# Kernel optimization log

Measured on AMD Instinct MI355X. Metric: run time of the kernel, lower is better.

## Reference

```python
import jax, jax.numpy as jnp
import numpy as np

NUM_HEADS = 16
BN_EPS = 1e-5


def setup_inputs() -> dict:
    key = jax.random.key(0)
    ks = jax.random.split(key, 12)
    B, S, D = 8, 1024, 1024
    s = 1.0 / np.sqrt(D)
    return {
        "key": jax.random.normal(ks[0], (B, S, D), jnp.float32),
        "value": jax.random.normal(ks[1], (B, S, D), jnp.float32),
        "query": jax.random.normal(ks[2], (B, S, D), jnp.float32),
        "Wk": jax.random.normal(ks[3], (D, D), jnp.float32) * s,
        "bk": jax.random.normal(ks[4], (D,), jnp.float32) * s,
        "Wv": jax.random.normal(ks[5], (D, D), jnp.float32) * s,
        "bv": jax.random.normal(ks[6], (D,), jnp.float32) * s,
        "Wq": jax.random.normal(ks[7], (D, D), jnp.float32) * s,
        "bq": jax.random.normal(ks[8], (D,), jnp.float32) * s,
        "Wf": jax.random.normal(ks[9], (D, D), jnp.float32) * s,
        "bf": jax.random.normal(ks[10], (D,), jnp.float32) * s,
        "gamma": jnp.ones((D,), jnp.float32),
        "beta": jnp.zeros((D,), jnp.float32),
    }


def _mha(key, value, query, Wk, bk, Wv, bv, Wq, bq, Wf, bf, gamma, beta):
    B, S, D = query.shape
    H = NUM_HEADS
    d = D // H
    residual = query

    k = key @ Wk + bk      # [B, S, D]
    v = value @ Wv + bv
    q = query @ Wq + bq

    # Faithful to torch: raw row-major view(B*H, -1, d) — NOT the standard head transpose.
    k = k.reshape(B * H, -1, d)   # [B*H, S, d]
    v = v.reshape(B * H, -1, d)
    q = q.reshape(B * H, -1, d)

    # Faithful quirky scale: (dim_per_head // num_heads) ** -0.5
    scale = jnp.float32((d // H) ** (-0.5))

    scores = jnp.einsum('bqd,bkd->bqk', q, k) * scale          # [B*H, S, S]
    attention = jax.nn.softmax(scores, axis=2)
    context = jnp.einsum('bqk,bkd->bqd', attention, v)          # [B*H, S, d]

    context = context.reshape(B, -1, D)                         # [B, S, D]
    out = context @ Wf + bf

    # BatchNorm1d over channel dim D (training mode: batch stats over B and S, biased var)
    x = residual + out                                          # [B, S, D]
    mean = jnp.mean(x, axis=(0, 1))
    var = jnp.mean((x - mean) ** 2, axis=(0, 1))
    out = (x - mean) * jax.lax.rsqrt(var + BN_EPS) * gamma + beta
    return out, attention


def reference(key, value, query, Wk, bk, Wv, bv, Wq, bq, Wf, bf, gamma, beta):
    return _mha(key, value, query, Wk, bk, Wv, bv, Wq, bq, Wf, bf, gamma, beta)
```

## Files before the change

### kernel.cpp

```cpp
#include <hip/hip_runtime.h>
#include <hip/hip_bf16.h>
#include <stdint.h>

typedef __attribute__((ext_vector_type(8))) short     short8;
typedef __attribute__((ext_vector_type(8))) _Float16  f16x8;
typedef __attribute__((ext_vector_type(4))) float     f32x4;
typedef __attribute__((ext_vector_type(8))) unsigned short ushort8;
typedef __attribute__((ext_vector_type(4))) unsigned short ushort4_t;

__device__ inline unsigned short f2bf(float f) {
    unsigned u = __float_as_uint(f);
    u += 0x7fffu + ((u >> 16) & 1u);
    return (unsigned short)(u >> 16);
}
__device__ inline float bf2f(unsigned short h) {
    return __uint_as_float(((unsigned)h) << 16);
}
__device__ inline unsigned short f2h(float f) {
    _Float16 h = (_Float16)f;
    unsigned short r;
    __builtin_memcpy(&r, &h, 2);
    return r;
}

__device__ inline void gload16(const void* g, void* lds) {
    unsigned loff = (unsigned)(uintptr_t)lds;
    loff = __builtin_amdgcn_readfirstlane(loff);
    auto l = (__attribute__((address_space(3))) unsigned int*)(uintptr_t)loff;
    auto p = (const __attribute__((address_space(1))) unsigned int*)(uintptr_t)g;
    __builtin_amdgcn_global_load_lds(p, l, 16, 0, 0);
}

template<int TOF16>
__global__ void cvt_f32_2b(const float4* __restrict__ in, ushort4_t* __restrict__ out, int n4) {
    for (int i = blockIdx.x * blockDim.x + threadIdx.x; i < n4; i += gridDim.x * blockDim.x) {
        float4 v = in[i];
        ushort4_t r;
        if constexpr (TOF16) { r.x = f2h(v.x);  r.y = f2h(v.y);  r.z = f2h(v.z);  r.w = f2h(v.w); }
        else                 { r.x = f2bf(v.x); r.y = f2bf(v.y); r.z = f2bf(v.z); r.w = f2bf(v.w); }
        out[i] = r;
    }
}

template<int TOF16>
__global__ void transpose_cvt(const float* __restrict__ W, unsigned short* __restrict__ WT, int dim) {
    __shared__ float t[32][33];
    const int bx = blockIdx.x * 32, by = blockIdx.y * 32;
    const int tx = threadIdx.x, ty = threadIdx.y;
#pragma unroll
    for (int i = 0; i < 4; ++i)
        t[ty + 8 * i][tx] = W[(size_t)(by + ty + 8 * i) * dim + bx + tx];
    __syncthreads();
#pragma unroll
    for (int i = 0; i < 4; ++i) {
        float v = t[tx][ty + 8 * i];
        WT[(size_t)(bx + ty + 8 * i) * dim + by + tx] = TOF16 ? f2h(v) : f2bf(v);
    }
}

__global__ void transpose_v(const unsigned short* __restrict__ v, unsigned short* __restrict__ vT) {
    const int bh = blockIdx.z, d0 = blockIdx.x * 32, s0 = blockIdx.y * 32;
    __shared__ unsigned short t[32][33];
    const int tx = threadIdx.x, ty = threadIdx.y;
    const size_t base = (size_t)bh << 16;
#pragma unroll
    for (int i = 0; i < 4; ++i)
        t[ty + 8 * i][tx] = v[base + (size_t)(s0 + ty + 8 * i) * 64 + d0 + tx];
    __syncthreads();
#pragma unroll
    for (int i = 0; i < 4; ++i)
        vT[base + (size_t)(d0 + ty + 8 * i) * 1024 + s0 + tx] = t[tx][ty + 8 * i];
}

template<int F16IN, int EPI>
__global__ __launch_bounds__(256, 2) void gemm_bt(
    const unsigned short* __restrict__ A,
    const unsigned short* __restrict__ Bt,
    const float* __restrict__ bias,
    unsigned short* __restrict__ C2b,
    const float* __restrict__ resid,
    float* __restrict__ Cf,
    int M, int N, int K, int nbx)
{
    const int bid = blockIdx.x;
    const int cpx = gridDim.x >> 3;
    const int swz = (bid & 7) * cpx + (bid >> 3);
    const int bm = swz / nbx, bn = swz % nbx;
    const int m0 = bm * 128, n0 = bn * 128;

    const int tid = threadIdx.x;
    const int w = tid >> 6, l = tid & 63, g = l >> 4, c = l & 15;
    const int wr = w >> 1, wc = w & 1;

    __shared__ unsigned short As[4096];
    __shared__ unsigned short Bs[4096];

    f32x4 acc[4][4] = {};

    const int arow = tid >> 2, acol = (tid & 3) * 8;
    const unsigned short* Ap  = A  + (size_t)(m0 + arow) * K + acol;
    const unsigned short* Ap2 = A  + (size_t)(m0 + 64 + arow) * K + acol;
    const unsigned short* Bp  = Bt + (size_t)(n0 + arow) * K + acol;
    const unsigned short* Bp2 = Bt + (size_t)(n0 + 64 + arow) * K + acol;
    unsigned short* AsW  = &As[w * 512];
    unsigned short* AsW2 = &As[2048 + w * 512];
    unsigned short* BsW  = &Bs[w * 512];
    unsigned short* BsW2 = &Bs[2048 + w * 512];

    for (int k0 = 0; k0 < K; k0 += 32) {
        gload16(Ap + k0,  AsW);
        gload16(Ap2 + k0, AsW2);
        gload16(Bp + k0,  BsW);
        gload16(Bp2 + k0, BsW2);
        asm volatile("s_waitcnt vmcnt(0)" ::: "memory");
        __syncthreads();

        if constexpr (F16IN) {
            f16x8 a[4], b[4];
#pragma unroll
            for (int mt = 0; mt < 4; ++mt)
                a[mt] = *(const f16x8*)&As[(wr * 64 + mt * 16 + c) * 32 + g * 8];
#pragma unroll
            for (int nt = 0; nt < 4; ++nt)
                b[nt] = *(const f16x8*)&Bs[(wc * 64 + nt * 16 + c) * 32 + g * 8];
#pragma unroll
            for (int mt = 0; mt < 4; ++mt)
#pragma unroll
                for (int nt = 0; nt < 4; ++nt)
                    acc[mt][nt] = __builtin_amdgcn_mfma_f32_16x16x32_f16(a[mt], b[nt], acc[mt][nt], 0, 0, 0);
        } else {
            short8 a[4], b[4];
#pragma unroll
            for (int mt = 0; mt < 4; ++mt)
                a[mt] = *(const short8*)&As[(wr * 64 + mt * 16 + c) * 32 + g * 8];
#pragma unroll
            for (int nt = 0; nt < 4; ++nt)
                b[nt] = *(const short8*)&Bs[(wc * 64 + nt * 16 + c) * 32 + g * 8];
#pragma unroll
            for (int mt = 0; mt < 4; ++mt)
#pragma unroll
                for (int nt = 0; nt < 4; ++nt)
                    acc[mt][nt] = __builtin_amdgcn_mfma_f32_16x16x32_bf16(a[mt], b[nt], acc[mt][nt], 0, 0, 0);
        }
        __syncthreads();
    }

#pragma unroll
    for (int nt = 0; nt < 4; ++nt) {
        const int col = n0 + wc * 64 + nt * 16 + c;
        const float bs = bias[col];
#pragma unroll
        for (int mt = 0; mt < 4; ++mt) {
            const int row0 = m0 + wr * 64 + mt * 16 + g * 4;
#pragma unroll
            for (int r = 0; r < 4; ++r) {
                const float x = acc[mt][nt][r] + bs;
                const size_t idx = (size_t)(row0 + r) * N + col;
                if constexpr (EPI == 0) {
                    C2b[idx] = F16IN ? f2h(x) : f2bf(x);
                } else {
                    Cf[idx] = x + resid[idx];
                }
            }
        }
    }
}

__global__ __launch_bounds__(256, 4) void attn_kernel(
    const unsigned short* __restrict__ qf,
    const unsigned short* __restrict__ kf,
    const unsigned short* __restrict__ vT,
    float* __restrict__ attn_out,
    unsigned short* __restrict__ ctx)
{
    const int rb = blockIdx.x;
    const int bh = blockIdx.y;
    const int tid = threadIdx.x;
    const int w = tid >> 6, l = tid & 63, g = l >> 4, c = l & 15;
    const int n0 = w * 256;

    __shared__ unsigned short P[16 * 1024];
    __shared__ float rs_lds[4][16];
    __shared__ float inv_lds[16];

    const unsigned short* qb = qf + ((size_t)bh << 16) + (size_t)(rb * 16 + c) * 64 + g * 8;
    const f16x8 q0 = *(const f16x8*)(qb);
    const f16x8 q1 = *(const f16x8*)(qb + 32);

    const unsigned short* kb = kf + ((size_t)bh << 16);
    const unsigned swzc = ((unsigned)(c & 7)) << 4;
    const unsigned prow = (unsigned)c * 2048;

    f32x4 pt[16];
    float rsum = 0.f;

#pragma unroll
    for (int t = 0; t < 16; ++t) {
        const unsigned short* kp = kb + (size_t)(n0 + t * 16 + c) * 64 + g * 8;
        const f16x8 a0 = *(const f16x8*)(kp);
        const f16x8 a1 = *(const f16x8*)(kp + 32);
        f32x4 s = {0.f, 0.f, 0.f, 0.f};
        s = __builtin_amdgcn_mfma_f32_16x16x32_f16(a0, q0, s, 0, 0, 0);
        s = __builtin_amdgcn_mfma_f32_16x16x32_f16(a1, q1, s, 0, 0, 0);

        f32x4 p;
        p[0] = __expf(s[0] * 0.5f);
        p[1] = __expf(s[1] * 0.5f);
        p[2] = __expf(s[2] * 0.5f);
        p[3] = __expf(s[3] * 0.5f);
        pt[t] = p;
        rsum += (p[0] + p[1]) + (p[2] + p[3]);

        ushort4_t pk;
        pk.x = f2bf(p[0]); pk.y = f2bf(p[1]); pk.z = f2bf(p[2]); pk.w = f2bf(p[3]);
        *(ushort4_t*)((char*)P + ((prow + (unsigned)(n0 * 2 + t * 32 + g * 8)) ^ swzc)) = pk;
    }

    rsum += __shfl_xor(rsum, 16);
    rsum += __shfl_xor(rsum, 32);
    if (g == 0) rs_lds[w][c] = rsum;
    __syncthreads();
    if (tid < 16)
        inv_lds[tid] = 1.0f / (rs_lds[0][tid] + rs_lds[1][tid] + rs_lds[2][tid] + rs_lds[3][tid]);
    __syncthreads();

    const float inv = inv_lds[c];
    float* ao = attn_out + ((size_t)bh << 20) + (size_t)(rb * 16 + c) * 1024 + n0 + g * 4;
#pragma unroll
    for (int t = 0; t < 16; ++t) {
        f32x4 o;
        o[0] = pt[t][0] * inv;
        o[1] = pt[t][1] * inv;
        o[2] = pt[t][2] * inv;
        o[3] = pt[t][3] * inv;
        __builtin_nontemporal_store(o, (f32x4*)(ao + t * 16));
    }

    f32x4 pacc = {0.f, 0.f, 0.f, 0.f};
    const unsigned short* vb = vT + ((size_t)bh << 16) + (size_t)(w * 16 + c) * 1024;
#pragma unroll 4
    for (int ks = 0; ks < 32; ++ks) {
        const short8 a = *(const short8*)((char*)P + ((prow + (unsigned)(ks * 64 + g * 16)) ^ swzc));
        const short8 b = *(const short8*)(vb + ks * 32 + g * 8);
        pacc = __builtin_amdgcn_mfma_f32_16x16x32_bf16(a, b, pacc, 0, 0, 0);
    }
    unsigned short* cb = ctx + ((size_t)bh << 16) + (size_t)(rb * 16) * 64 + w * 16 + c;
#pragma unroll
    for (int r = 0; r < 4; ++r) {
        const int row = g * 4 + r;
        cb[(size_t)row * 64] = f2bf(pacc[r] * inv_lds[row]);
    }
}

__global__ void bn_stats(const float* __restrict__ x, float* __restrict__ psum, float* __restrict__ psq) {
    const int col = blockIdx.y * 256 + threadIdx.x;
    const int r0 = blockIdx.x * 128;
    float s = 0.f, q = 0.f;
#pragma unroll 4
    for (int r = 0; r < 128; ++r) {
        const float v = x[(size_t)(r0 + r) * 1024 + col];
        s += v; q += v * v;
    }
    psum[blockIdx.x * 1024 + col] = s;
    psq [blockIdx.x * 1024 + col] = q;
}

__global__ void bn_final(const float* __restrict__ psum, const float* __restrict__ psq,
                         const float* __restrict__ gamma, const float* __restrict__ beta,
                         float* __restrict__ ab) {
    const int cidx = threadIdx.x;
    float s = 0.f, q = 0.f;
#pragma unroll 8
    for (int i = 0; i < 64; ++i) { s += psum[i * 1024 + cidx]; q += psq[i * 1024 + cidx]; }
    const float mean = s * (1.0f / 8192.0f);
    const float var  = q * (1.0f / 8192.0f) - mean * mean;
    const float a = gamma[cidx] * rsqrtf(var + 1e-5f);
    ab[cidx]        = a;
    ab[1024 + cidx] = beta[cidx] - mean * a;
}

__global__ void bn_apply(const float4* __restrict__ x4, const float* __restrict__ ab, float4* __restrict__ o4) {
    const int n4 = 2 * 1024 * 1024;
    for (int i = blockIdx.x * blockDim.x + threadIdx.x; i < n4; i += gridDim.x * blockDim.x) {
        const float4 v = x4[i];
        const int c0 = (i & 255) << 2;
        float4 r;
        r.x = v.x * ab[c0 + 0] + ab[1024 + c0 + 0];
        r.y = v.y * ab[c0 + 1] + ab[1024 + c0 + 1];
        r.z = v.z * ab[c0 + 2] + ab[1024 + c0 + 2];
        r.w = v.w * ab[c0 + 3] + ab[1024 + c0 + 3];
        o4[i] = r;
    }
}

extern "C" void kernel_launch(void* const* d_in, const int* in_sizes, int n_in,
                              void* d_out, int out_size, void* d_ws, size_t ws_size,
                              hipStream_t stream) {
    (void)in_sizes; (void)n_in; (void)out_size; (void)ws_size;

    const float* key   = (const float*)d_in[0];
    const float* value = (const float*)d_in[1];
    const float* query = (const float*)d_in[2];
    const float* Wk = (const float*)d_in[3];
    const float* bk = (const float*)d_in[4];
    const float* Wv = (const float*)d_in[5];
    const float* bv = (const float*)d_in[6];
    const float* Wq = (const float*)d_in[7];
    const float* bq = (const float*)d_in[8];
    const float* Wf = (const float*)d_in[9];
    const float* bff = (const float*)d_in[10];
    const float* gamma = (const float*)d_in[11];
    const float* beta  = (const float*)d_in[12];

    char* ws = (char*)d_ws;
    const size_t MB = 1u << 20;
    unsigned short* key16   = (unsigned short*)(ws + 0);
    unsigned short* ctx     = (unsigned short*)(ws + 0);
    unsigned short* query16 = (unsigned short*)(ws + 16 * MB);
    unsigned short* value16 = (unsigned short*)(ws + 32 * MB);
    float*          xbuf    = (float*)(ws + 16 * MB);
    unsigned short* WkT = (unsigned short*)(ws + 48 * MB);
    unsigned short* WqT = (unsigned short*)(ws + 50 * MB);
    unsigned short* WvT = (unsigned short*)(ws + 52 * MB);
    unsigned short* WfT = (unsigned short*)(ws + 54 * MB);
    unsigned short* kbuf = (unsigned short*)(ws + 56 * MB);
    unsigned short* qbuf = (unsigned short*)(ws + 72 * MB);
    unsigned short* vbuf = (unsigned short*)(ws + 88 * MB);
    float* psum = (float*)(ws + 88 * MB);
    float* psq  = (float*)(ws + 88 * MB + 256 * 1024);
    float* ab   = (float*)(ws + 88 * MB + 512 * 1024);
    unsigned short* vTbuf = (unsigned short*)(ws + 104 * MB);

    float* out0 = (float*)d_out;
    float* attn = out0 + 8388608;

    const int n4big = 2 * 1024 * 1024;

    cvt_f32_2b<1><<<2048, 256, 0, stream>>>((const float4*)key,   (ushort4_t*)key16,   n4big);
    cvt_f32_2b<1><<<2048, 256, 0, stream>>>((const float4*)query, (ushort4_t*)query16, n4big);
    cvt_f32_2b<0><<<2048, 256, 0, stream>>>((const float4*)value, (ushort4_t*)value16, n4big);

    dim3 tb(32, 8), tg(32, 32);
    transpose_cvt<1><<<tg, tb, 0, stream>>>(Wk, WkT, 1024);
    transpose_cvt<1><<<tg, tb, 0, stream>>>(Wq, WqT, 1024);
    transpose_cvt<0><<<tg, tb, 0, stream>>>(Wv, WvT, 1024);
    transpose_cvt<0><<<tg, tb, 0, stream>>>(Wf, WfT, 1024);

    gemm_bt<1, 0><<<512, 256, 0, stream>>>(key16,   WkT, bk, kbuf, nullptr, nullptr, 8192, 1024, 1024, 8);
    gemm_bt<1, 0><<<512, 256, 0, stream>>>(query16, WqT, bq, qbuf, nullptr, nullptr, 8192, 1024, 1024, 8);
    gemm_bt<0, 0><<<512, 256, 0, stream>>>(value16, WvT, bv, vbuf, nullptr, nullptr, 8192, 1024, 1024, 8);

    transpose_v<<<dim3(2, 32, 128), tb, 0, stream>>>(vbuf, vTbuf);

    attn_kernel<<<dim3(64, 128), 256, 0, stream>>>(qbuf, kbuf, vTbuf, attn, ctx);

    gemm_bt<0, 1><<<512, 256, 0, stream>>>(ctx, WfT, bff, nullptr, query, xbuf, 8192, 1024, 1024, 8);

    bn_stats<<<dim3(64, 4), 256, 0, stream>>>(xbuf, psum, psq);
    bn_final<<<1, 1024, 0, stream>>>(psum, psq, gamma, beta, ab);
    bn_apply<<<2048, 256, 0, stream>>>((const float4*)xbuf, ab, (float4*)out0);
}
```

Before: 471.7 us.

## Merge input conversions, remap attention grid for L2 locality, reorder PV before stores

```diff
diff --git a/kernel.cpp b/kernel.cpp
--- a/kernel.cpp
+++ b/kernel.cpp
@@ -31,13 +31,19 @@
     __builtin_amdgcn_global_load_lds(p, l, 16, 0, 0);
 }
 
-template<int TOF16>
-__global__ void cvt_f32_2b(const float4* __restrict__ in, ushort4_t* __restrict__ out, int n4) {
+__global__ void cvt3_f32_2b(const float4* __restrict__ k, const float4* __restrict__ q,
+                            const float4* __restrict__ v,
+                            ushort4_t* __restrict__ k16, ushort4_t* __restrict__ q16,
+                            ushort4_t* __restrict__ v16, int n4) {
+    const int which = blockIdx.y;
+    const float4* in  = which == 0 ? k   : which == 1 ? q   : v;
+    ushort4_t*    out = which == 0 ? k16 : which == 1 ? q16 : v16;
+    const bool tof16 = (which < 2);
     for (int i = blockIdx.x * blockDim.x + threadIdx.x; i < n4; i += gridDim.x * blockDim.x) {
-        float4 v = in[i];
+        float4 vv = in[i];
         ushort4_t r;
-        if constexpr (TOF16) { r.x = f2h(v.x);  r.y = f2h(v.y);  r.z = f2h(v.z);  r.w = f2h(v.w); }
-        else                 { r.x = f2bf(v.x); r.y = f2bf(v.y); r.z = f2bf(v.z); r.w = f2bf(v.w); }
+        if (tof16) { r.x = f2h(vv.x);  r.y = f2h(vv.y);  r.z = f2h(vv.z);  r.w = f2h(vv.w); }
+        else       { r.x = f2bf(vv.x); r.y = f2bf(vv.y); r.z = f2bf(vv.z); r.w = f2bf(vv.w); }
         out[i] = r;
     }
 }
@@ -173,8 +179,10 @@
     float* __restrict__ attn_out,
     unsigned short* __restrict__ ctx)
 {
-    const int rb = blockIdx.x;
-    const int bh = blockIdx.y;
+    const int L = blockIdx.x;
+    const int rb = (L >> 3) & 63;
+    const int bh = ((L & 7) << 4) | (L >> 9);
+
     const int tid = threadIdx.x;
     const int w = tid >> 6, l = tid & 63, g = l >> 4, c = l & 15;
     const int n0 = w * 256;
@@ -224,6 +232,23 @@
         inv_lds[tid] = 1.0f / (rs_lds[0][tid] + rs_lds[1][tid] + rs_lds[2][tid] + rs_lds[3][tid]);
     __syncthreads();
 
+    f32x4 pacc = {0.f, 0.f, 0.f, 0.f};
+    const unsigned short* vb = vT + ((size_t)bh << 16) + (size_t)(w * 16 + c) * 1024;
+    __builtin_amdgcn_s_setprio(1);
+#pragma unroll 4
+    for (int ks = 0; ks < 32; ++ks) {
+        const short8 a = *(const short8*)((char*)P + ((prow + (unsigned)(ks * 64 + g * 16)) ^ swzc));
+        const short8 b = *(const short8*)(vb + ks * 32 + g * 8);
+        pacc = __builtin_amdgcn_mfma_f32_16x16x32_bf16(a, b, pacc, 0, 0, 0);
+    }
+    __builtin_amdgcn_s_setprio(0);
+    unsigned short* cb = ctx + ((size_t)bh << 16) + (size_t)(rb * 16) * 64 + w * 16 + c;
+#pragma unroll
+    for (int r = 0; r < 4; ++r) {
+        const int row = g * 4 + r;
+        cb[(size_t)row * 64] = f2bf(pacc[r] * inv_lds[row]);
+    }
+
     const float inv = inv_lds[c];
     float* ao = attn_out + ((size_t)bh << 20) + (size_t)(rb * 16 + c) * 1024 + n0 + g * 4;
 #pragma unroll
@@ -234,21 +259,6 @@
         o[2] = pt[t][2] * inv;
         o[3] = pt[t][3] * inv;
         __builtin_nontemporal_store(o, (f32x4*)(ao + t * 16));
-    }
-
-    f32x4 pacc = {0.f, 0.f, 0.f, 0.f};
-    const unsigned short* vb = vT + ((size_t)bh << 16) + (size_t)(w * 16 + c) * 1024;
-#pragma unroll 4
-    for (int ks = 0; ks < 32; ++ks) {
-        const short8 a = *(const short8*)((char*)P + ((prow + (unsigned)(ks * 64 + g * 16)) ^ swzc));
-        const short8 b = *(const short8*)(vb + ks * 32 + g * 8);
-        pacc = __builtin_amdgcn_mfma_f32_16x16x32_bf16(a, b, pacc, 0, 0, 0);
-    }
-    unsigned short* cb = ctx + ((size_t)bh << 16) + (size_t)(rb * 16) * 64 + w * 16 + c;
-#pragma unroll
-    for (int r = 0; r < 4; ++r) {
-        const int row = g * 4 + r;
-        cb[(size_t)row * 64] = f2bf(pacc[r] * inv_lds[row]);
     }
 }
 
@@ -336,9 +346,9 @@
 
     const int n4big = 2 * 1024 * 1024;
 
-    cvt_f32_2b<1><<<2048, 256, 0, stream>>>((const float4*)key,   (ushort4_t*)key16,   n4big);
-    cvt_f32_2b<1><<<2048, 256, 0, stream>>>((const float4*)query, (ushort4_t*)query16, n4big);
-    cvt_f32_2b<0><<<2048, 256, 0, stream>>>((const float4*)value, (ushort4_t*)value16, n4big);
+    cvt3_f32_2b<<<dim3(1024, 3), 256, 0, stream>>>(
+        (const float4*)key, (const float4*)query, (const float4*)value,
+        (ushort4_t*)key16, (ushort4_t*)query16, (ushort4_t*)value16, n4big);
 
     dim3 tb(32, 8), tg(32, 32);
     transpose_cvt<1><<<tg, tb, 0, stream>>>(Wk, WkT, 1024);
@@ -352,7 +362,7 @@
 
     transpose_v<<<dim3(2, 32, 128), tb, 0, stream>>>(vbuf, vTbuf);
 
-    attn_kernel<<<dim3(64, 128), 256, 0, stream>>>(qbuf, kbuf, vTbuf, attn, ctx);
+    attn_kernel<<<8192, 256, 0, stream>>>(qbuf, kbuf, vTbuf, attn, ctx);
 
     gemm_bt<0, 1><<<512, 256, 0, stream>>>(ctx, WfT, bff, nullptr, query, xbuf, 8192, 1024, 1024, 8);
 
```

After: 495.1 us. +4.9%, slower.
